# Performance work log

Hardware: AMD Instinct MI355X
Metric: run time of the kernel (lower is better)

Reference implementation:

```python
import jax, jax.numpy as jnp
import numpy as np

jax.config.update("jax_enable_x64", True)

# config
B, S = 4, 4096
H_SIZE = 2048          # hidden_size
VOCAB = 128000         # engram_base_vocab_size
MAX_NGRAM = 3          # engram_max_ngram_size -> orders 2..3
PRIME = 500009         # engram_n_embed_per_ngram (same prime for every order)
N_HEAD = 4             # engram_n_head_per_ngram
E = 32                 # engram_embed_dim
KS = 4                 # short conv kernel size
NUM_ORDERS = MAX_NGRAM - 1
TOTAL_HEADS = NUM_ORDERS * N_HEAD
TOTAL_ROWS = PRIME * N_HEAD * NUM_ORDERS  # flat multi-head table rows


def setup_inputs() -> dict:
    key = jax.random.key(0)
    k_ids, k_h, k_tab, k_cw, k_hp, k_gp, k_op = jax.random.split(key, 7)
    input_ids = jax.random.randint(k_ids, (B, S), 0, VOCAB, dtype=jnp.int64)
    hidden_states = jax.random.normal(k_h, (B, S, H_SIZE), dtype=jnp.float32)
    # identity compressed-tokenizer mapping buffer
    mapping = jnp.arange(VOCAB, dtype=jnp.int64)
    # deterministic odd multipliers, seeded like _build_multipliers
    rng = np.random.default_rng(0 * 10007 + 0 * 1009)
    mults = rng.integers(1, 2 ** 31, size=(NUM_ORDERS, N_HEAD, MAX_NGRAM))
    multipliers = jnp.asarray(mults * 2 + 1, dtype=jnp.int64)
    table = 0.02 * jax.random.normal(k_tab, (TOTAL_ROWS, E), dtype=jnp.float32)
    conv_w = 0.1 * jax.random.normal(k_cw, (E, KS), dtype=jnp.float32)  # depthwise taps
    conv_b = jnp.zeros((E,), dtype=jnp.float32)
    Wh = 0.05 * jax.random.normal(k_hp, (E, TOTAL_HEADS * E), dtype=jnp.float32)
    Wg = 0.02 * jax.random.normal(k_gp, (E, H_SIZE), dtype=jnp.float32)
    Wo = 0.02 * jax.random.normal(k_op, (H_SIZE, E), dtype=jnp.float32)
    return {"input_ids": input_ids, "hidden_states": hidden_states,
            "mapping": mapping, "multipliers": multipliers, "table": table,
            "conv_w": conv_w, "conv_b": conv_b, "Wh": Wh, "Wg": Wg, "Wo": Wo}


def _hash_indices(compressed, multipliers):
    """XOR-mix n-gram hash indices -> [B, S, TOTAL_HEADS] int64."""
    all_idx = []
    offset = 0
    for oi, k in enumerate(range(2, MAX_NGRAM + 1)):
        # forward sliding window, clamped at last token (matches cat/expand trick)
        pos = jnp.minimum(jnp.arange(S)[:, None] + jnp.arange(k)[None, :], S - 1)  # [S,k]
        ng = compressed[:, pos]                                  # [B,S,k]
        m = multipliers[oi, :, :k]                               # [nh,k]
        prod = ng[:, :, None, :] * m[None, None, :, :]           # [B,S,nh,k]
        h = prod[..., 0]
        for p in range(1, k):
            h = h ^ prod[..., p]
        idx = h % PRIME + (offset + jnp.arange(N_HEAD, dtype=jnp.int64) * PRIME)
        all_idx.append(idx)
        offset += PRIME * N_HEAD
    return jnp.concatenate(all_idx, axis=-1)


def reference(input_ids, hidden_states, mapping, multipliers, table,
              conv_w, conv_b, Wh, Wg, Wo):
    compressed = mapping[input_ids]                              # [B,S]
    indices = _hash_indices(compressed, multipliers)             # [B,S,TOTAL_HEADS]
    emb = table[indices].reshape(B, S, TOTAL_HEADS * E)          # multi-head gather
    emb = emb @ Wh.T                                             # head_proj -> [B,S,E]
    # causal depthwise short conv (kernel KS, left pad KS-1)
    xp = jnp.pad(emb, ((0, 0), (KS - 1, 0), (0, 0)))
    emb = sum(xp[:, j:j + S, :] * conv_w[:, j] for j in range(KS)) + conv_b
    gate = jax.nn.sigmoid(hidden_states @ Wg.T)                  # [B,S,E]
    return (gate * emb) @ Wo.T                                   # [B,S,H_SIZE]
```

## Files before the change

kernel.cpp:

```cpp
#include <hip/hip_runtime.h>
#include <hip/hip_bf16.h>
#include <stdint.h>

#define HSZ 2048
#define PRIME 500009u

typedef __attribute__((ext_vector_type(8))) short short8;
typedef __attribute__((ext_vector_type(4))) float f32x4;
typedef __attribute__((ext_vector_type(4))) unsigned uint4v;
typedef __attribute__((ext_vector_type(2))) unsigned uint2v;

__device__ __forceinline__ unsigned pk2(float x, float y) {
  __hip_bfloat162 h = __float22bfloat162_rn(make_float2(x, y));
  return *reinterpret_cast<unsigned*>(&h);
}
__device__ __forceinline__ short f2bf(float f) {
  __hip_bfloat16 h = __float2bfloat16(f);
  return *reinterpret_cast<short*>(&h);
}

__device__ __forceinline__ short8 load8_bf(const float* __restrict__ p) {
  float4 a = *reinterpret_cast<const float4*>(p);
  float4 b = *reinterpret_cast<const float4*>(p + 4);
  uint4v u = {pk2(a.x, a.y), pk2(a.z, a.w), pk2(b.x, b.y), pk2(b.z, b.w)};
  return __builtin_bit_cast(short8, u);
}

__global__ __launch_bounds__(256) void emb0_kernel(
    const int* __restrict__ ids, const int* __restrict__ mapping,
    const unsigned* __restrict__ mult, const float* __restrict__ table,
    const float* __restrict__ Wh, float* __restrict__ emb0) {
  __shared__ __align__(16) short A_lds[32][264];
  __shared__ int idx_lds[256];
  const int tid = threadIdx.x;
  const int t0 = blockIdx.x * 32;

  {
    int t_loc = tid >> 3, head = tid & 7;
    int tg = t0 + t_loc;
    int b = tg >> 12, s = tg & 4095;
    const int* idb = ids + (b << 12);
    int s1 = s + 1 > 4095 ? 4095 : s + 1;
    int s2 = s + 2 > 4095 ? 4095 : s + 2;
    uint64_t c0 = (unsigned)mapping[idb[s]];
    uint64_t c1 = (unsigned)mapping[idb[s1]];
    uint64_t c2 = (unsigned)mapping[idb[s2]];
    int mb = head * 3;
    uint64_t h = (c0 * (uint64_t)mult[mb]) ^ (c1 * (uint64_t)mult[mb + 1]);
    if (head >= 4) h ^= c2 * (uint64_t)mult[mb + 2];
    unsigned row = (unsigned)(h % PRIME) + (unsigned)head * PRIME;
    idx_lds[tid] = (int)row;
  }
  __syncthreads();

  #pragma unroll
  for (int p = 0; p < 8; ++p) {
    int r = p * 32 + (tid >> 3);
    int c4 = (tid & 7) * 4;
    long row = idx_lds[r];
    float4 v = *reinterpret_cast<const float4*>(table + row * 32 + c4);
    int tl = r >> 3, hd = r & 7;
    uint2v pk = {pk2(v.x, v.y), pk2(v.z, v.w)};
    *reinterpret_cast<uint2v*>(&A_lds[tl][hd * 32 + c4]) = pk;
  }
  __syncthreads();

  int wid = tid >> 6, lane = tid & 63;
  int tt = wid >> 1, e0 = (wid & 1) * 16;
  int l16 = lane & 15, q = lane >> 4;
  short8 Wf[8];
  #pragma unroll
  for (int ks = 0; ks < 8; ++ks)
    Wf[ks] = load8_bf(Wh + (size_t)(e0 + l16) * 256 + ks * 32 + q * 8);
  f32x4 acc = {0.f, 0.f, 0.f, 0.f};
  #pragma unroll
  for (int ks = 0; ks < 8; ++ks) {
    short8 a = *reinterpret_cast<const short8*>(&A_lds[tt * 16 + l16][ks * 32 + q * 8]);
    acc = __builtin_amdgcn_mfma_f32_16x16x32_bf16(Wf[ks], a, acc, 0, 0, 0);
  }
  int t = t0 + tt * 16 + l16;
  *reinterpret_cast<f32x4*>(&emb0[(size_t)t * 32 + e0 + q * 4]) = acc;
}

__global__ __launch_bounds__(256) void fuse_kernel(
    const float* __restrict__ hidden, const float* __restrict__ emb0,
    const float* __restrict__ cw, const float* __restrict__ cb,
    const float* __restrict__ Wg, const float* __restrict__ Wo,
    float* __restrict__ out) {
  __shared__ float emb_lds[32][33];
  __shared__ __align__(16) short ge_lds[32][40];
  __shared__ float accred[2][64][8];
  const int tid = threadIdx.x;
  const int t0 = blockIdx.x * 32;

  #pragma unroll
  for (int it = 0; it < 4; ++it) {
    int ii = it * 256 + tid;
    int tl = ii >> 5, e = ii & 31;
    int s = (t0 + tl) & 4095;
    float a = cb[e];
    #pragma unroll
    for (int j = 0; j < 4; ++j) {
      int sp = s - 3 + j;
      if (sp >= 0) a += cw[e * 4 + j] * emb0[(size_t)(t0 + tl - 3 + j) * 32 + e];
    }
    emb_lds[tl][e] = a;
  }

  int wid = tid >> 6, lane = tid & 63;
  int l16 = lane & 15, q = lane >> 4;
  int tt = wid & 1, kh = wid >> 1;

  f32x4 acc0 = {0, 0, 0, 0}, acc1 = {0, 0, 0, 0};
  const float* hrow = hidden + (size_t)(t0 + tt * 16 + l16) * HSZ + kh * 1024 + q * 8;
  const float* wg0 = Wg + (size_t)l16 * HSZ + kh * 1024 + q * 8;
  const float* wg1 = Wg + (size_t)(16 + l16) * HSZ + kh * 1024 + q * 8;
  for (int kc = 0; kc < 4; ++kc) {
    short8 B0[8], B1[8];
    #pragma unroll
    for (int ks = 0; ks < 8; ++ks) {
      B0[ks] = load8_bf(wg0 + kc * 256 + ks * 32);
      B1[ks] = load8_bf(wg1 + kc * 256 + ks * 32);
    }
    #pragma unroll
    for (int ks = 0; ks < 8; ++ks) {
      short8 a = load8_bf(hrow + kc * 256 + ks * 32);
      acc0 = __builtin_amdgcn_mfma_f32_16x16x32_bf16(a, B0[ks], acc0, 0, 0, 0);
      acc1 = __builtin_amdgcn_mfma_f32_16x16x32_bf16(a, B1[ks], acc1, 0, 0, 0);
    }
  }
  if (kh == 1) {
    #pragma unroll
    for (int j = 0; j < 4; ++j) {
      accred[tt][lane][j] = acc0[j];
      accred[tt][lane][4 + j] = acc1[j];
    }
  }
  __syncthreads();
  if (kh == 0) {
    #pragma unroll
    for (int j = 0; j < 4; ++j) {
      acc0[j] += accred[tt][lane][j];
      acc1[j] += accred[tt][lane][4 + j];
    }
    #pragma unroll
    for (int j = 0; j < 4; ++j) {
      int r = tt * 16 + q * 4 + j;
      float g0 = 1.f / (1.f + __expf(-acc0[j]));
      ge_lds[r][l16] = f2bf(g0 * emb_lds[r][l16]);
      float g1 = 1.f / (1.f + __expf(-acc1[j]));
      ge_lds[r][16 + l16] = f2bf(g1 * emb_lds[r][16 + l16]);
    }
  }
  __syncthreads();

  short8 Af0 = *reinterpret_cast<const short8*>(&ge_lds[l16][q * 8]);
  short8 Af1 = *reinterpret_cast<const short8*>(&ge_lds[16 + l16][q * 8]);
  float* orow0 = out + (size_t)(t0 + l16) * HSZ;
  float* orow1 = out + (size_t)(t0 + 16 + l16) * HSZ;
  int hbase = wid * 512;
  for (int ht = 0; ht < 32; ++ht) {
    int h0 = hbase + ht * 16;
    short8 aw = load8_bf(Wo + (size_t)(h0 + l16) * 32 + q * 8);
    f32x4 z = {0, 0, 0, 0};
    f32x4 o0 = __builtin_amdgcn_mfma_f32_16x16x32_bf16(aw, Af0, z, 0, 0, 0);
    f32x4 o1 = __builtin_amdgcn_mfma_f32_16x16x32_bf16(aw, Af1, z, 0, 0, 0);
    *reinterpret_cast<f32x4*>(orow0 + h0 + q * 4) = o0;
    *reinterpret_cast<f32x4*>(orow1 + h0 + q * 4) = o1;
  }
}

extern "C" void kernel_launch(void* const* d_in, const int* in_sizes, int n_in,
                              void* d_out, int out_size, void* d_ws, size_t ws_size,
                              hipStream_t stream) {
  const int* ids = (const int*)d_in[0];
  const float* hidden = (const float*)d_in[1];
  const int* mapping = (const int*)d_in[2];
  const unsigned* mult = (const unsigned*)d_in[3];
  const float* table = (const float*)d_in[4];
  const float* cw = (const float*)d_in[5];
  const float* cb = (const float*)d_in[6];
  const float* Wh = (const float*)d_in[7];
  const float* Wg = (const float*)d_in[8];
  const float* Wo = (const float*)d_in[9];
  float* out = (float*)d_out;
  float* emb0 = (float*)d_ws;

  emb0_kernel<<<512, 256, 0, stream>>>(ids, mapping, mult, table, Wh, emb0);
  fuse_kernel<<<512, 256, 0, stream>>>(hidden, emb0, cw, cb, Wg, Wo, out);
}
```

Baseline: 92.70 us.

## Stage hidden tiles via async global-to-LDS loads with double buffering

In fuse_kernel, the hidden-state rows are copied into a swizzled, double-buffered LDS tile with global_load_lds, so the next K chunk loads while MFMAs run on the current one. The gate GEMM's work split changes from a K-split across waves (with an LDS reduction) to each wave owning 16 output columns over the full K. This aims to hide global-load latency on the dominant hidden-state stream. In exchange it uses 64KB of LDS per block, which lowers occupancy, and adds a barrier per K chunk.

```diff
diff --git a/kernel.cpp b/kernel.cpp
--- a/kernel.cpp
+++ b/kernel.cpp
@@ -18,12 +18,19 @@
   __hip_bfloat16 h = __float2bfloat16(f);
   return *reinterpret_cast<short*>(&h);
 }
-
+__device__ __forceinline__ short8 pack8(float4 a, float4 b) {
+  uint4v u = {pk2(a.x, a.y), pk2(a.z, a.w), pk2(b.x, b.y), pk2(b.z, b.w)};
+  return __builtin_bit_cast(short8, u);
+}
 __device__ __forceinline__ short8 load8_bf(const float* __restrict__ p) {
   float4 a = *reinterpret_cast<const float4*>(p);
   float4 b = *reinterpret_cast<const float4*>(p + 4);
-  uint4v u = {pk2(a.x, a.y), pk2(a.z, a.w), pk2(b.x, b.y), pk2(b.z, b.w)};
-  return __builtin_bit_cast(short8, u);
+  return pack8(a, b);
+}
+__device__ __forceinline__ void gload_lds16(const float* g, void* l) {
+  __builtin_amdgcn_global_load_lds(
+      (const __attribute__((address_space(1))) void*)g,
+      (__attribute__((address_space(3))) void*)l, 16, 0, 0);
 }
 
 __global__ __launch_bounds__(256) void emb0_kernel(
@@ -87,11 +94,25 @@
     const float* __restrict__ cw, const float* __restrict__ cb,
     const float* __restrict__ Wg, const float* __restrict__ Wo,
     float* __restrict__ out) {
+  __shared__ __align__(16) float hbuf[2][32][256];
   __shared__ float emb_lds[32][33];
   __shared__ __align__(16) short ge_lds[32][40];
-  __shared__ float accred[2][64][8];
   const int tid = threadIdx.x;
+  const int wid = tid >> 6, lane = tid & 63;
+  const int l16 = lane & 15, q = lane >> 4;
   const int t0 = blockIdx.x * 32;
+
+  auto STAGE = [&](int buf, int kc) {
+    #pragma unroll
+    for (int j = 0; j < 8; ++j) {
+      int r = wid * 8 + j;
+      unsigned so = ((unsigned)(lane * 16) ^ (((unsigned)r & 7) << 4)) >> 2;
+      const float* src = hidden + (size_t)(t0 + r) * HSZ + kc * 256 + so;
+      gload_lds16(src, &hbuf[buf][r][0]);
+    }
+  };
+
+  STAGE(0, 0);
 
   #pragma unroll
   for (int it = 0; it < 4; ++it) {
@@ -106,51 +127,38 @@
     }
     emb_lds[tl][e] = a;
   }
+  __syncthreads();
 
-  int wid = tid >> 6, lane = tid & 63;
-  int l16 = lane & 15, q = lane >> 4;
-  int tt = wid & 1, kh = wid >> 1;
-
-  f32x4 acc0 = {0, 0, 0, 0}, acc1 = {0, 0, 0, 0};
-  const float* hrow = hidden + (size_t)(t0 + tt * 16 + l16) * HSZ + kh * 1024 + q * 8;
-  const float* wg0 = Wg + (size_t)l16 * HSZ + kh * 1024 + q * 8;
-  const float* wg1 = Wg + (size_t)(16 + l16) * HSZ + kh * 1024 + q * 8;
-  for (int kc = 0; kc < 4; ++kc) {
-    short8 B0[8], B1[8];
+  const int tt = wid >> 1, ee = wid & 1;
+  const int R = tt * 16 + l16;
+  const unsigned sw = ((unsigned)R & 7) << 4;
+  const char* hrow0 = (const char*)&hbuf[0][0][0] + R * 1024;
+  const char* hrow1 = (const char*)&hbuf[1][0][0] + R * 1024;
+  const float* wgp = Wg + (size_t)(ee * 16 + l16) * HSZ + q * 8;
+  f32x4 acc = {0.f, 0.f, 0.f, 0.f};
+  for (int kc = 0; kc < 8; ++kc) {
+    if (kc < 7) STAGE((kc + 1) & 1, kc + 1);
+    const char* hb = (kc & 1) ? hrow1 : hrow0;
+    short8 A[8], B[8];
     #pragma unroll
     for (int ks = 0; ks < 8; ++ks) {
-      B0[ks] = load8_bf(wg0 + kc * 256 + ks * 32);
-      B1[ks] = load8_bf(wg1 + kc * 256 + ks * 32);
+      B[ks] = load8_bf(wgp + kc * 256 + ks * 32);
+      unsigned b0 = (unsigned)(ks * 128 + q * 32);
+      float4 a0 = *reinterpret_cast<const float4*>(hb + (b0 ^ sw));
+      float4 a1 = *reinterpret_cast<const float4*>(hb + ((b0 + 16) ^ sw));
+      A[ks] = pack8(a0, a1);
     }
     #pragma unroll
-    for (int ks = 0; ks < 8; ++ks) {
-      short8 a = load8_bf(hrow + kc * 256 + ks * 32);
-      acc0 = __builtin_amdgcn_mfma_f32_16x16x32_bf16(a, B0[ks], acc0, 0, 0, 0);
-      acc1 = __builtin_amdgcn_mfma_f32_16x16x32_bf16(a, B1[ks], acc1, 0, 0, 0);
-    }
+    for (int ks = 0; ks < 8; ++ks)
+      acc = __builtin_amdgcn_mfma_f32_16x16x32_bf16(A[ks], B[ks], acc, 0, 0, 0);
+    __syncthreads();
   }
-  if (kh == 1) {
-    #pragma unroll
-    for (int j = 0; j < 4; ++j) {
-      accred[tt][lane][j] = acc0[j];
-      accred[tt][lane][4 + j] = acc1[j];
-    }
-  }
-  __syncthreads();
-  if (kh == 0) {
-    #pragma unroll
-    for (int j = 0; j < 4; ++j) {
-      acc0[j] += accred[tt][lane][j];
-      acc1[j] += accred[tt][lane][4 + j];
-    }
-    #pragma unroll
-    for (int j = 0; j < 4; ++j) {
-      int r = tt * 16 + q * 4 + j;
-      float g0 = 1.f / (1.f + __expf(-acc0[j]));
-      ge_lds[r][l16] = f2bf(g0 * emb_lds[r][l16]);
-      float g1 = 1.f / (1.f + __expf(-acc1[j]));
-      ge_lds[r][16 + l16] = f2bf(g1 * emb_lds[r][16 + l16]);
-    }
+
+  #pragma unroll
+  for (int j = 0; j < 4; ++j) {
+    int r = tt * 16 + q * 4 + j, c = ee * 16 + l16;
+    float g = 1.f / (1.f + __expf(-acc[j]));
+    ge_lds[r][c] = f2bf(g * emb_lds[r][c]);
   }
   __syncthreads();
 
```

New measurement: 90.78 us. 2.1% less time.
